# Kernel tuning notes

Measured on AMD Instinct MI355X. Metric: run time of the kernel, lower is better.

Reference implementation:

```python
import jax, jax.numpy as jnp
import numpy as np

# Hardcoded capability requirements per task (3 capabilities x 13 tasks), as in the source.
CAP_MATRIX = 0.01 * np.array([
    [0.0, 33.0, 50.0, 43.0, 56.0, 67.0, 62.0, 47.0, 50.0, 51.0, 64.0, 64.0, 68.0],
    [0.0, 33.0, 49.0, 39.0, 58.0, 67.0, 60.0, 54.0, 52.0, 52.0, 67.0, 69.0, 71.0],
    [0.0, 33.0, 42.0, 39.0, 44.0, 52.0, 49.0, 42.0, 45.0, 46.0, 52.0, 53.0, 56.0],
], dtype=np.float32)  # [3, 13]

T_TASKS = 64      # tasks per observation sequence
B_SEQS = 262144   # number of observation sequences
N_TASK_IDS = 13
CAP_DIM = 3


def setup_inputs() -> dict:
    key = jax.random.key(0)
    k1, k2, k3, k4, k5 = jax.random.split(key, 5)
    # Performance encoding must avoid the invalid (1,1) combo:
    # state 0 -> (0,0) no info; state 1 -> (0,1) success; state 2 -> (1,0) failure.
    state = jax.random.randint(k1, (T_TASKS, B_SEQS), 0, 3)
    inptasksperf = jnp.stack(
        [(state == 2).astype(jnp.int32), (state == 1).astype(jnp.int32)], axis=-1
    )  # [T, B, 2]
    tasksobsids = jax.random.randint(k2, (T_TASKS, B_SEQS, 1), 0, N_TASK_IDS).astype(jnp.int32)
    taskspredids = jax.random.randint(k3, (B_SEQS, 1), 0, N_TASK_IDS).astype(jnp.int32)
    inptasksobs = jnp.zeros((T_TASKS, B_SEQS, 1), jnp.float32)  # only shapes are used
    betas = 20.0 * jax.random.uniform(k4, (CAP_DIM,), jnp.float32)
    zetas = jax.random.uniform(k5, (CAP_DIM,), jnp.float32)
    return {
        "inptasksobs": inptasksobs,
        "inptasksperf": inptasksperf,
        "tasksobsids": tasksobsids,
        "taskspredids": taskspredids,
        "num_obs_tasks": T_TASKS,
        "betas": betas,
        "zetas": zetas,
    }


def reference(inptasksobs, inptasksperf, tasksobsids, taskspredids, num_obs_tasks, betas, zetas):
    cap_table = jnp.asarray(CAP_MATRIX.T)                # [13, 3] per-task capability rows
    obs_cap = cap_table[tasksobsids[..., 0]]             # [T, B, 3]
    p0 = inptasksperf[..., 0] != 0                       # [T, B]
    p1 = inptasksperf[..., 1] != 0
    success = jnp.logical_and(~p0, p1)                   # (0,1) -> success
    failure = jnp.logical_and(p0, ~p1)                   # (1,0) -> failure; (0,0) -> skip

    def step(cap, x):
        oc, s, f = x                                     # oc [B,3], s/f [B]
        cap = jnp.where(s[:, None], jnp.maximum(cap, oc), cap)
        cap = jnp.where(f[:, None], jnp.minimum(cap, oc), cap)
        return cap, None

    cap0 = jnp.zeros((obs_cap.shape[1], CAP_DIM), jnp.float32)
    cap, _ = jax.lax.scan(step, cap0, (obs_cap, success, failure))  # [B, 3]

    req = cap_table[taskspredids[:, 0]]                  # [B, 3]
    p = betas * (req - cap)                              # [B, 3]
    trust = jnp.prod((1.0 + jnp.exp(p)) ** (-zetas), axis=-1, keepdims=True)  # [B, 1]
    return trust
```

## Files before the change

kernel.cpp:

```cpp
#include <hip/hip_runtime.h>

#define T_TASKS 64
#define B_SEQS 262144

__constant__ float c_capT[13 * 3] = {
    0.01f *  0.0f, 0.01f *  0.0f, 0.01f *  0.0f,
    0.01f * 33.0f, 0.01f * 33.0f, 0.01f * 33.0f,
    0.01f * 50.0f, 0.01f * 49.0f, 0.01f * 42.0f,
    0.01f * 43.0f, 0.01f * 39.0f, 0.01f * 39.0f,
    0.01f * 56.0f, 0.01f * 58.0f, 0.01f * 44.0f,
    0.01f * 67.0f, 0.01f * 67.0f, 0.01f * 52.0f,
    0.01f * 62.0f, 0.01f * 60.0f, 0.01f * 49.0f,
    0.01f * 47.0f, 0.01f * 54.0f, 0.01f * 42.0f,
    0.01f * 50.0f, 0.01f * 52.0f, 0.01f * 45.0f,
    0.01f * 51.0f, 0.01f * 52.0f, 0.01f * 46.0f,
    0.01f * 64.0f, 0.01f * 67.0f, 0.01f * 52.0f,
    0.01f * 64.0f, 0.01f * 69.0f, 0.01f * 53.0f,
    0.01f * 68.0f, 0.01f * 71.0f, 0.01f * 56.0f,
};

__global__ __launch_bounds__(256) void trust_kernel(
    const int2* __restrict__ perf,
    const int*  __restrict__ obsids,
    const int*  __restrict__ predids,
    const float* __restrict__ betas,
    const float* __restrict__ zetas,
    float* __restrict__ out)
{
    __shared__ float s_cap[13 * 3];
    if (threadIdx.x < 13 * 3) s_cap[threadIdx.x] = c_capT[threadIdx.x];
    __syncthreads();

    const int b = blockIdx.x * blockDim.x + threadIdx.x;

    float c0 = 0.0f, c1 = 0.0f, c2 = 0.0f;
    const int2* pp = perf + b;
    const int*  op = obsids + b;

    #pragma unroll 8
    for (int t = 0; t < T_TASKS; ++t) {
        const int2 pf = pp[(size_t)t * B_SEQS];
        const int  id = op[(size_t)t * B_SEQS];
        const float o0 = s_cap[id * 3 + 0];
        const float o1 = s_cap[id * 3 + 1];
        const float o2 = s_cap[id * 3 + 2];
        const bool p0 = (pf.x != 0);
        const bool p1 = (pf.y != 0);
        const bool su = (!p0) && p1;
        const bool fa = p0 && (!p1);
        c0 = su ? fmaxf(c0, o0) : (fa ? fminf(c0, o0) : c0);
        c1 = su ? fmaxf(c1, o1) : (fa ? fminf(c1, o1) : c1);
        c2 = su ? fmaxf(c2, o2) : (fa ? fminf(c2, o2) : c2);
    }

    const int pid = predids[b];
    const float r0 = s_cap[pid * 3 + 0];
    const float r1 = s_cap[pid * 3 + 1];
    const float r2 = s_cap[pid * 3 + 2];

    const float q0 = betas[0] * (r0 - c0);
    const float q1 = betas[1] * (r1 - c1);
    const float q2 = betas[2] * (r2 - c2);

    const float t0 = powf(1.0f + expf(q0), -zetas[0]);
    const float t1 = powf(1.0f + expf(q1), -zetas[1]);
    const float t2 = powf(1.0f + expf(q2), -zetas[2]);

    out[b] = t0 * t1 * t2;
}

extern "C" void kernel_launch(void* const* d_in, const int* in_sizes, int n_in,
                              void* d_out, int out_size, void* d_ws, size_t ws_size,
                              hipStream_t stream) {
    const int2*  perf    = (const int2*)d_in[1];
    const int*   obsids  = (const int*)d_in[2];
    const int*   predids = (const int*)d_in[3];
    const float* betas   = (const float*)d_in[5];
    const float* zetas   = (const float*)d_in[6];
    float* out = (float*)d_out;

    const int threads = 256;
    const int blocks  = B_SEQS / threads;
    trust_kernel<<<blocks, threads, 0, stream>>>(perf, obsids, predids, betas, zetas, out);
}
```

Baseline: 269.0 us.

## Split time scan into parallel chunks composed via clamp-function summaries

Each block now covers 64 sequences with 4 threads per sequence. Each thread scans a 16-step chunk and summarizes it as a clamp function (low/high bounds), with all its loads issued up front. The chunk summaries are combined in shared memory by composing the clamps, then applied to the initial zero capability. This exposes more memory-level parallelism on a bandwidth-bound scan, at the cost of extra min/max work and a block barrier, and only a quarter of the threads run the epilogue.

```diff
diff --git a/kernel.cpp b/kernel.cpp
--- a/kernel.cpp
+++ b/kernel.cpp
@@ -2,6 +2,13 @@
 
 #define T_TASKS 64
 #define B_SEQS 262144
+#define CHUNKS 4
+#define OBS_PER_CHUNK 16
+#define SEQ_PER_BLOCK 64
+#define BLOCK 256
+
+#define POS_BIG  3.402823466e+38f
+#define NEG_BIG -3.402823466e+38f
 
 __constant__ float c_capT[13 * 3] = {
     0.01f *  0.0f, 0.01f *  0.0f, 0.01f *  0.0f,
@@ -19,7 +26,7 @@
     0.01f * 68.0f, 0.01f * 71.0f, 0.01f * 56.0f,
 };
 
-__global__ __launch_bounds__(256) void trust_kernel(
+__global__ __launch_bounds__(BLOCK) void trust_kernel(
     const int2* __restrict__ perf,
     const int*  __restrict__ obsids,
     const int*  __restrict__ predids,
@@ -28,45 +35,80 @@
     float* __restrict__ out)
 {
     __shared__ float s_cap[13 * 3];
+    __shared__ float s_lh[CHUNKS][SEQ_PER_BLOCK][6];
     if (threadIdx.x < 13 * 3) s_cap[threadIdx.x] = c_capT[threadIdx.x];
     __syncthreads();
 
-    const int b = blockIdx.x * blockDim.x + threadIdx.x;
+    const int lane = threadIdx.x & (SEQ_PER_BLOCK - 1);
+    const int c    = threadIdx.x >> 6;
+    const int b    = blockIdx.x * SEQ_PER_BLOCK + lane;
 
-    float c0 = 0.0f, c1 = 0.0f, c2 = 0.0f;
-    const int2* pp = perf + b;
-    const int*  op = obsids + b;
+    const size_t base = (size_t)(c * OBS_PER_CHUNK) * B_SEQS + (size_t)b;
+    int2 pfa[OBS_PER_CHUNK];
+    int  ida[OBS_PER_CHUNK];
+    #pragma unroll
+    for (int t = 0; t < OBS_PER_CHUNK; ++t) {
+        pfa[t] = perf[base + (size_t)t * B_SEQS];
+        ida[t] = obsids[base + (size_t)t * B_SEQS];
+    }
 
-    #pragma unroll 8
-    for (int t = 0; t < T_TASKS; ++t) {
-        const int2 pf = pp[(size_t)t * B_SEQS];
-        const int  id = op[(size_t)t * B_SEQS];
+    float l0 = NEG_BIG, l1 = NEG_BIG, l2 = NEG_BIG;
+    float h0 = POS_BIG, h1 = POS_BIG, h2 = POS_BIG;
+    #pragma unroll
+    for (int t = 0; t < OBS_PER_CHUNK; ++t) {
+        const int   id = ida[t];
         const float o0 = s_cap[id * 3 + 0];
         const float o1 = s_cap[id * 3 + 1];
         const float o2 = s_cap[id * 3 + 2];
-        const bool p0 = (pf.x != 0);
-        const bool p1 = (pf.y != 0);
+        const bool p0 = (pfa[t].x != 0);
+        const bool p1 = (pfa[t].y != 0);
         const bool su = (!p0) && p1;
         const bool fa = p0 && (!p1);
-        c0 = su ? fmaxf(c0, o0) : (fa ? fminf(c0, o0) : c0);
-        c1 = su ? fmaxf(c1, o1) : (fa ? fminf(c1, o1) : c1);
-        c2 = su ? fmaxf(c2, o2) : (fa ? fminf(c2, o2) : c2);
+        l0 = su ? fmaxf(l0, o0) : (fa ? fminf(l0, o0) : l0);
+        h0 = su ? fmaxf(h0, o0) : (fa ? fminf(h0, o0) : h0);
+        l1 = su ? fmaxf(l1, o1) : (fa ? fminf(l1, o1) : l1);
+        h1 = su ? fmaxf(h1, o1) : (fa ? fminf(h1, o1) : h1);
+        l2 = su ? fmaxf(l2, o2) : (fa ? fminf(l2, o2) : l2);
+        h2 = su ? fmaxf(h2, o2) : (fa ? fminf(h2, o2) : h2);
     }
 
-    const int pid = predids[b];
-    const float r0 = s_cap[pid * 3 + 0];
-    const float r1 = s_cap[pid * 3 + 1];
-    const float r2 = s_cap[pid * 3 + 2];
+    float* p = &s_lh[c][lane][0];
+    p[0] = l0; p[1] = l1; p[2] = l2;
+    p[3] = h0; p[4] = h1; p[5] = h2;
+    __syncthreads();
 
-    const float q0 = betas[0] * (r0 - c0);
-    const float q1 = betas[1] * (r1 - c1);
-    const float q2 = betas[2] * (r2 - c2);
+    if (threadIdx.x < SEQ_PER_BLOCK) {
+        const int sl = threadIdx.x;
+        float L0 = s_lh[0][sl][0], L1 = s_lh[0][sl][1], L2 = s_lh[0][sl][2];
+        float H0 = s_lh[0][sl][3], H1 = s_lh[0][sl][4], H2 = s_lh[0][sl][5];
+        #pragma unroll
+        for (int cc = 1; cc < CHUNKS; ++cc) {
+            const float lc0 = s_lh[cc][sl][0], lc1 = s_lh[cc][sl][1], lc2 = s_lh[cc][sl][2];
+            const float hc0 = s_lh[cc][sl][3], hc1 = s_lh[cc][sl][4], hc2 = s_lh[cc][sl][5];
+            L0 = fminf(fmaxf(L0, lc0), hc0);  H0 = fminf(fmaxf(H0, lc0), hc0);
+            L1 = fminf(fmaxf(L1, lc1), hc1);  H1 = fminf(fmaxf(H1, lc1), hc1);
+            L2 = fminf(fmaxf(L2, lc2), hc2);  H2 = fminf(fmaxf(H2, lc2), hc2);
+        }
+        const float c0 = fminf(fmaxf(0.0f, L0), H0);
+        const float c1 = fminf(fmaxf(0.0f, L1), H1);
+        const float c2 = fminf(fmaxf(0.0f, L2), H2);
 
-    const float t0 = powf(1.0f + expf(q0), -zetas[0]);
-    const float t1 = powf(1.0f + expf(q1), -zetas[1]);
-    const float t2 = powf(1.0f + expf(q2), -zetas[2]);
+        const int bb  = blockIdx.x * SEQ_PER_BLOCK + sl;
+        const int pid = predids[bb];
+        const float r0 = s_cap[pid * 3 + 0];
+        const float r1 = s_cap[pid * 3 + 1];
+        const float r2 = s_cap[pid * 3 + 2];
 
-    out[b] = t0 * t1 * t2;
+        const float q0 = betas[0] * (r0 - c0);
+        const float q1 = betas[1] * (r1 - c1);
+        const float q2 = betas[2] * (r2 - c2);
+
+        const float t0 = powf(1.0f + expf(q0), -zetas[0]);
+        const float t1 = powf(1.0f + expf(q1), -zetas[1]);
+        const float t2 = powf(1.0f + expf(q2), -zetas[2]);
+
+        out[bb] = t0 * t1 * t2;
+    }
 }
 
 extern "C" void kernel_launch(void* const* d_in, const int* in_sizes, int n_in,
@@ -79,7 +121,6 @@
     const float* zetas   = (const float*)d_in[6];
     float* out = (float*)d_out;
 
-    const int threads = 256;
-    const int blocks  = B_SEQS / threads;
-    trust_kernel<<<blocks, threads, 0, stream>>>(perf, obsids, predids, betas, zetas, out);
+    const int blocks = B_SEQS / SEQ_PER_BLOCK;
+    trust_kernel<<<blocks, BLOCK, 0, stream>>>(perf, obsids, predids, betas, zetas, out);
 }
```

New measurement: 268.7 us. About the same (-0.1%).

## Split scan across threads via clamp composition with vectorized prefetched loads

Applied to the files above, without the earlier changes.

Treats each max/min update as a clamp and uses fmed3 to accumulate a composed [lo,hi] clamp. Two half-blocks each process half of the time steps, and the halves are merged through shared memory. Each thread handles two sequences using int4/int2 loads, with an 8-deep register prefetch to raise memory-level parallelism. The merge adds a shared-memory pass and leaves half the threads idle during the final transcendental math.

```diff
diff --git a/kernel.cpp b/kernel.cpp
--- a/kernel.cpp
+++ b/kernel.cpp
@@ -2,84 +2,144 @@
 
 #define T_TASKS 64
 #define B_SEQS 262144
+#define BLOCK 256
+#define HALF_T 32
+#define DEPTH 8
 
-__constant__ float c_capT[13 * 3] = {
-    0.01f *  0.0f, 0.01f *  0.0f, 0.01f *  0.0f,
-    0.01f * 33.0f, 0.01f * 33.0f, 0.01f * 33.0f,
-    0.01f * 50.0f, 0.01f * 49.0f, 0.01f * 42.0f,
-    0.01f * 43.0f, 0.01f * 39.0f, 0.01f * 39.0f,
-    0.01f * 56.0f, 0.01f * 58.0f, 0.01f * 44.0f,
-    0.01f * 67.0f, 0.01f * 67.0f, 0.01f * 52.0f,
-    0.01f * 62.0f, 0.01f * 60.0f, 0.01f * 49.0f,
-    0.01f * 47.0f, 0.01f * 54.0f, 0.01f * 42.0f,
-    0.01f * 50.0f, 0.01f * 52.0f, 0.01f * 45.0f,
-    0.01f * 51.0f, 0.01f * 52.0f, 0.01f * 46.0f,
-    0.01f * 64.0f, 0.01f * 67.0f, 0.01f * 52.0f,
-    0.01f * 64.0f, 0.01f * 69.0f, 0.01f * 53.0f,
-    0.01f * 68.0f, 0.01f * 71.0f, 0.01f * 56.0f,
+#define POS_BIG  3.402823466e+38f
+#define NEG_BIG -3.402823466e+38f
+
+__constant__ float c_capT[13][4] = {
+    {0.00f, 0.00f, 0.00f, 0.f}, {0.33f, 0.33f, 0.33f, 0.f},
+    {0.50f, 0.49f, 0.42f, 0.f}, {0.43f, 0.39f, 0.39f, 0.f},
+    {0.56f, 0.58f, 0.44f, 0.f}, {0.67f, 0.67f, 0.52f, 0.f},
+    {0.62f, 0.60f, 0.49f, 0.f}, {0.47f, 0.54f, 0.42f, 0.f},
+    {0.50f, 0.52f, 0.45f, 0.f}, {0.51f, 0.52f, 0.46f, 0.f},
+    {0.64f, 0.67f, 0.52f, 0.f}, {0.64f, 0.69f, 0.53f, 0.f},
+    {0.68f, 0.71f, 0.56f, 0.f},
 };
 
-__global__ __launch_bounds__(256) void trust_kernel(
-    const int2* __restrict__ perf,
-    const int*  __restrict__ obsids,
-    const int*  __restrict__ predids,
+#define STEP(l, h, A, B)                          \
+    l = __builtin_amdgcn_fmed3f(l, A, B);         \
+    h = __builtin_amdgcn_fmed3f(h, A, B);
+
+__global__ __launch_bounds__(BLOCK) void trust_kernel(
+    const int4* __restrict__ perf2,
+    const int2* __restrict__ obs2,
+    const int2* __restrict__ pred2,
     const float* __restrict__ betas,
     const float* __restrict__ zetas,
-    float* __restrict__ out)
+    float2* __restrict__ out2)
 {
-    __shared__ float s_cap[13 * 3];
-    if (threadIdx.x < 13 * 3) s_cap[threadIdx.x] = c_capT[threadIdx.x];
+    __shared__ float4 s_cap[13];
+    __shared__ float  s_lh[2][128][13];
+
+    if (threadIdx.x < 13)
+        s_cap[threadIdx.x] = *(const float4*)&c_capT[threadIdx.x][0];
     __syncthreads();
 
-    const int b = blockIdx.x * blockDim.x + threadIdx.x;
+    const int tid = threadIdx.x;
+    const int c   = tid >> 7;
+    const int pr  = tid & 127;
+    const size_t pair      = (size_t)blockIdx.x * 128 + pr;
+    const size_t rowStride = B_SEQS / 2;
+    const size_t base      = (size_t)(c * HALF_T) * rowStride + pair;
 
-    float c0 = 0.0f, c1 = 0.0f, c2 = 0.0f;
-    const int2* pp = perf + b;
-    const int*  op = obsids + b;
-
-    #pragma unroll 8
-    for (int t = 0; t < T_TASKS; ++t) {
-        const int2 pf = pp[(size_t)t * B_SEQS];
-        const int  id = op[(size_t)t * B_SEQS];
-        const float o0 = s_cap[id * 3 + 0];
-        const float o1 = s_cap[id * 3 + 1];
-        const float o2 = s_cap[id * 3 + 2];
-        const bool p0 = (pf.x != 0);
-        const bool p1 = (pf.y != 0);
-        const bool su = (!p0) && p1;
-        const bool fa = p0 && (!p1);
-        c0 = su ? fmaxf(c0, o0) : (fa ? fminf(c0, o0) : c0);
-        c1 = su ? fmaxf(c1, o1) : (fa ? fminf(c1, o1) : c1);
-        c2 = su ? fmaxf(c2, o2) : (fa ? fminf(c2, o2) : c2);
+    int4 pfa[DEPTH];
+    int2 ida[DEPTH];
+    #pragma unroll
+    for (int i = 0; i < DEPTH; ++i) {
+        pfa[i] = perf2[base + (size_t)i * rowStride];
+        ida[i] = obs2 [base + (size_t)i * rowStride];
     }
 
-    const int pid = predids[b];
-    const float r0 = s_cap[pid * 3 + 0];
-    const float r1 = s_cap[pid * 3 + 1];
-    const float r2 = s_cap[pid * 3 + 2];
+    float la0=NEG_BIG, la1=NEG_BIG, la2=NEG_BIG;
+    float ha0=POS_BIG, ha1=POS_BIG, ha2=POS_BIG;
+    float lb0=NEG_BIG, lb1=NEG_BIG, lb2=NEG_BIG;
+    float hb0=POS_BIG, hb1=POS_BIG, hb2=POS_BIG;
 
-    const float q0 = betas[0] * (r0 - c0);
-    const float q1 = betas[1] * (r1 - c1);
-    const float q2 = betas[2] * (r2 - c2);
+    #pragma unroll
+    for (int t = 0; t < HALF_T; ++t) {
+        const int  slot = t & (DEPTH - 1);
+        const int4 pf = pfa[slot];
+        const int2 id = ida[slot];
+        if (t + DEPTH < HALF_T) {
+            pfa[slot] = perf2[base + (size_t)(t + DEPTH) * rowStride];
+            ida[slot] = obs2 [base + (size_t)(t + DEPTH) * rowStride];
+        }
+        const float4 oa = s_cap[id.x];
+        const float4 ob = s_cap[id.y];
+        const bool sa = (pf.x == 0) && (pf.y != 0);
+        const bool fa = (pf.x != 0) && (pf.y == 0);
+        const bool sb = (pf.z == 0) && (pf.w != 0);
+        const bool fb = (pf.z != 0) && (pf.w == 0);
 
-    const float t0 = powf(1.0f + expf(q0), -zetas[0]);
-    const float t1 = powf(1.0f + expf(q1), -zetas[1]);
-    const float t2 = powf(1.0f + expf(q2), -zetas[2]);
+        const float Aa0 = sa ? oa.x : NEG_BIG, Ba0 = fa ? oa.x : POS_BIG;
+        const float Aa1 = sa ? oa.y : NEG_BIG, Ba1 = fa ? oa.y : POS_BIG;
+        const float Aa2 = sa ? oa.z : NEG_BIG, Ba2 = fa ? oa.z : POS_BIG;
+        const float Ab0 = sb ? ob.x : NEG_BIG, Bb0 = fb ? ob.x : POS_BIG;
+        const float Ab1 = sb ? ob.y : NEG_BIG, Bb1 = fb ? ob.y : POS_BIG;
+        const float Ab2 = sb ? ob.z : NEG_BIG, Bb2 = fb ? ob.z : POS_BIG;
 
-    out[b] = t0 * t1 * t2;
+        STEP(la0, ha0, Aa0, Ba0)
+        STEP(la1, ha1, Aa1, Ba1)
+        STEP(la2, ha2, Aa2, Ba2)
+        STEP(lb0, hb0, Ab0, Bb0)
+        STEP(lb1, hb1, Ab1, Bb1)
+        STEP(lb2, hb2, Ab2, Bb2)
+    }
+
+    float* dst = &s_lh[c][pr][0];
+    dst[0]=la0; dst[1]=la1; dst[2]=la2; dst[3]=ha0; dst[4]=ha1; dst[5]=ha2;
+    dst[6]=lb0; dst[7]=lb1; dst[8]=lb2; dst[9]=hb0; dst[10]=hb1; dst[11]=hb2;
+    __syncthreads();
+
+    if (tid < 128) {
+        const float* q0 = &s_lh[0][tid][0];
+        const float* q1 = &s_lh[1][tid][0];
+
+        float ca0 = fminf(fmaxf(0.0f, q0[0]), q0[3]);
+        float ca1 = fminf(fmaxf(0.0f, q0[1]), q0[4]);
+        float ca2 = fminf(fmaxf(0.0f, q0[2]), q0[5]);
+        ca0 = fminf(fmaxf(ca0, q1[0]), q1[3]);
+        ca1 = fminf(fmaxf(ca1, q1[1]), q1[4]);
+        ca2 = fminf(fmaxf(ca2, q1[2]), q1[5]);
+
+        float cb0 = fminf(fmaxf(0.0f, q0[6]), q0[9]);
+        float cb1 = fminf(fmaxf(0.0f, q0[7]), q0[10]);
+        float cb2 = fminf(fmaxf(0.0f, q0[8]), q0[11]);
+        cb0 = fminf(fmaxf(cb0, q1[6]), q1[9]);
+        cb1 = fminf(fmaxf(cb1, q1[7]), q1[10]);
+        cb2 = fminf(fmaxf(cb2, q1[8]), q1[11]);
+
+        const size_t pair = (size_t)blockIdx.x * 128 + tid;
+        const int2 pid = pred2[pair];
+        const float4 ra = s_cap[pid.x];
+        const float4 rb = s_cap[pid.y];
+        const float be0 = betas[0], be1 = betas[1], be2 = betas[2];
+        const float ze0 = zetas[0], ze1 = zetas[1], ze2 = zetas[2];
+
+        const float ta = powf(1.0f + expf(be0 * (ra.x - ca0)), -ze0)
+                       * powf(1.0f + expf(be1 * (ra.y - ca1)), -ze1)
+                       * powf(1.0f + expf(be2 * (ra.z - ca2)), -ze2);
+        const float tb = powf(1.0f + expf(be0 * (rb.x - cb0)), -ze0)
+                       * powf(1.0f + expf(be1 * (rb.y - cb1)), -ze1)
+                       * powf(1.0f + expf(be2 * (rb.z - cb2)), -ze2);
+
+        out2[pair] = make_float2(ta, tb);
+    }
 }
 
 extern "C" void kernel_launch(void* const* d_in, const int* in_sizes, int n_in,
                               void* d_out, int out_size, void* d_ws, size_t ws_size,
                               hipStream_t stream) {
-    const int2*  perf    = (const int2*)d_in[1];
-    const int*   obsids  = (const int*)d_in[2];
-    const int*   predids = (const int*)d_in[3];
-    const float* betas   = (const float*)d_in[5];
-    const float* zetas   = (const float*)d_in[6];
-    float* out = (float*)d_out;
+    const int4*  perf2 = (const int4*)d_in[1];
+    const int2*  obs2  = (const int2*)d_in[2];
+    const int2*  pred2 = (const int2*)d_in[3];
+    const float* betas = (const float*)d_in[5];
+    const float* zetas = (const float*)d_in[6];
+    float2* out2 = (float2*)d_out;
 
-    const int threads = 256;
-    const int blocks  = B_SEQS / threads;
-    trust_kernel<<<blocks, threads, 0, stream>>>(perf, obsids, predids, betas, zetas, out);
+    const int blocks = B_SEQS / 256;
+    trust_kernel<<<blocks, BLOCK, 0, stream>>>(perf2, obs2, pred2, betas, zetas, out2);
 }
```

Result: no change. 268.0 us (-0.4%).
